# Kernel optimization log

Measured on AMD Instinct MI355X. Metric: run time of the kernel, lower is better.

The kernel has to match this reference:

```python
import jax, jax.numpy as jnp
import jax.lax as lax
import numpy as np

X_NUM = 512
Y_NUM = 512
GRID = 1.0 / 512.0
MIN_X = 0.0
MIN_Y = 0.0
N_POINTS = 400000
BATCH = 4
NUM_CLASSES = 20


def setup_inputs():
    key = jax.random.key(0)
    ks = jax.random.split(key, 32)
    # rows 0/1: x,y coords in [0,1) so they land inside the 512x512 grid; rows 2-5: features
    xy = jax.random.uniform(ks[0], (2, N_POINTS), jnp.float32, 0.0, 1.0 - 1e-6)
    feat = jax.random.normal(ks[1], (4, N_POINTS), jnp.float32) * 0.5
    points = jnp.concatenate([xy, feat], 0)
    batch_ids = jax.random.randint(ks[2], (N_POINTS,), 0, BATCH, jnp.int32)
    inp = {"batch_ids": batch_ids, "points": points, "batch_size": BATCH}

    def lin(k, o, i):
        return jax.random.normal(k, (o, i), jnp.float32) * (1.0 / np.sqrt(i))

    ki = 3
    # pointwise conv1d stacks: (name, out_ch, in_ch)
    for name, o, i in [("0", 16, 6), ("1", 16, 16), ("v0", 16, 18), ("v1", 16, 32), ("2", 32, 32)]:
        inp["w" + name] = lin(ks[ki], o, i); ki += 1
        inp["b" + name] = jnp.zeros((o,), jnp.float32)
        inp["s" + name] = jax.random.uniform(ks[ki], (o,), jnp.float32, 0.5, 1.5); ki += 1
        inp["t" + name] = jax.random.normal(ks[ki], (o,), jnp.float32) * 0.1; ki += 1
    inp["w2d"] = jax.random.normal(ks[ki], (4, 32, 32, 3, 3), jnp.float32) * (1.0 / np.sqrt(32 * 9)); ki += 1
    inp["b2d"] = jnp.zeros((4, 32), jnp.float32)
    inp["s2d"] = jax.random.uniform(ks[ki], (4, 32), jnp.float32, 0.5, 1.5); ki += 1
    inp["t2d"] = jax.random.normal(ks[ki], (4, 32), jnp.float32) * 0.1; ki += 1
    inp["w3"] = lin(ks[ki], NUM_CLASSES, 64); ki += 1
    inp["b3"] = jnp.zeros((NUM_CLASSES,), jnp.float32)
    return inp


def _pconv(x, w, b, s, t):
    # 1x1 conv1d + BatchNorm(inference affine) + ReLU; x: [Cin, N]
    return jax.nn.relu((w @ x + b[:, None]) * s[:, None] + t[:, None])


def _scatter_max(v, gids, n):
    # v: [C, N] -> [C, n]; empty segments filled with 0 (torch_scatter fill_value=0,
    # and all scattered values here are post-ReLU >= 0)
    seg = jax.ops.segment_max(v.T, gids, num_segments=n).T
    return jnp.where(jnp.isneginf(seg), 0.0, seg)


def _bilinear(img, ix, iy):
    # grid_sample(align_corners=False, padding zeros) in pixel coords; img: [C, H, W]
    C, H, W = img.shape
    x0 = jnp.floor(ix); y0 = jnp.floor(iy)
    wx = ix - x0; wy = iy - y0
    x0i = x0.astype(jnp.int32); y0i = y0.astype(jnp.int32)

    def tap(yi, xi):
        valid = ((yi >= 0) & (yi < H) & (xi >= 0) & (xi < W)).astype(img.dtype)
        return img[:, jnp.clip(yi, 0, H - 1), jnp.clip(xi, 0, W - 1)] * valid

    return (tap(y0i, x0i) * (1 - wx) * (1 - wy) + tap(y0i, x0i + 1) * wx * (1 - wy)
            + tap(y0i + 1, x0i) * (1 - wx) * wy + tap(y0i + 1, x0i + 1) * wx * wy)


def _forward(batch_ids, points, batch_size, w0, b0, s0, t0, w1, b1, s1, t1,
             wv0, bv0, sv0, tv0, wv1, bv1, sv1, tv1, w2, b2, s2, t2,
             w2d, b2d, s2d, t2d, w3, b3):
    x_g = jnp.floor((points[0] - MIN_X) / GRID).astype(jnp.int32)
    y_g = jnp.floor((points[1] - MIN_Y) / GRID).astype(jnp.int32)
    gids = batch_ids.astype(jnp.int32) * (X_NUM * Y_NUM) + y_g * X_NUM + x_g
    grid_num = batch_size * Y_NUM * X_NUM

    h = _pconv(points, w0, b0, s0, t0)       # [16, N]
    h = _pconv(h, w1, b1, s1, t1)            # [16, N]
    vx = (x_g.astype(jnp.float32) + 0.5) * GRID + MIN_X
    vy = (y_g.astype(jnp.float32) + 0.5) * GRID + MIN_Y
    h = jnp.concatenate([h, (points[0] - vx)[None], (points[1] - vy)[None]], 0)  # [18, N]

    # VFE blocks: pointwise conv -> scatter_max over voxel ids -> gather back -> concat
    o = _pconv(h, wv0, bv0, sv0, tv0)        # [16, N]
    h = jnp.concatenate([o, _scatter_max(o, gids, grid_num)[:, gids]], 0)  # [32, N]
    o = _pconv(h, wv1, bv1, sv1, tv1)        # [16, N]
    h = jnp.concatenate([o, _scatter_max(o, gids, grid_num)[:, gids]], 0)  # [32, N]

    point0 = _pconv(h, w2, b2, s2, t2)       # [32, N]
    grid = _scatter_max(point0, gids, grid_num)
    grid = grid.reshape(32, batch_size, Y_NUM, X_NUM).transpose(1, 0, 2, 3)  # [B,32,Y,X]

    for i in range(4):
        p = 1 if i == 0 else 2
        grid = lax.conv_general_dilated(grid, w2d[i], (1, 1), ((p, p), (p, p)),
                                        rhs_dilation=(p, p),
                                        dimension_numbers=("NCHW", "OIHW", "NCHW"))
        grid = jax.nn.relu((grid + b2d[i][None, :, None, None]) * s2d[i][None, :, None, None]
                           + t2d[i][None, :, None, None])

    # interpolate (grid_sample) back to points; pixel coords reduce to (x-MIN)/GRID - 1
    img = grid.transpose(1, 0, 2, 3).reshape(32, batch_size * Y_NUM, X_NUM)
    ix = (points[0] - MIN_X) / GRID - 1.0
    iy = (points[1] - MIN_Y) / GRID - 1.0 + batch_ids.astype(jnp.float32) * Y_NUM
    point1 = _bilinear(img, ix, iy)          # [32, N]

    point = jnp.concatenate([point0, point1], 0)  # [64, N]
    return w3 @ point + b3[:, None]               # [num_classes, N]


def reference(batch_ids, points, batch_size, w0, b0, s0, t0, w1, b1, s1, t1,
              wv0, bv0, sv0, tv0, wv1, bv1, sv1, tv1, w2, b2, s2, t2,
              w2d, b2d, s2d, t2d, w3, b3):
    return _forward(batch_ids, points, batch_size, w0, b0, s0, t0, w1, b1, s1, t1,
                    wv0, bv0, sv0, tv0, wv1, bv1, sv1, tv1, w2, b2, s2, t2,
                    w2d, b2d, s2d, t2d, w3, b3)
```

## Files before the change

kernel.cpp:

```cpp
#include <hip/hip_runtime.h>
#include <hip/hip_bf16.h>
#include <hip/hip_fp16.h>

#define N_PTS 400000
#define XN 512
#define YN 512
#define BATCHN 4
#define VOX (XN*YN)
#define GRID_NUM (BATCHN*VOX)

typedef unsigned long long u64;
typedef __attribute__((ext_vector_type(8))) _Float16 f16x8;
typedef __attribute__((ext_vector_type(4))) float f32x4;

static __device__ __forceinline__ float relu_(float x){ return fmaxf(x, 0.0f); }
static __device__ __forceinline__ int voxel_id(float px, float py, int b){
    int xg = (int)floorf(px*512.0f);
    int yg = (int)floorf(py*512.0f);
    return b*VOX + yg*XN + xg;
}

static __device__ __forceinline__ u64 packh4(const float* v){
    u64 r = 0;
    #pragma unroll
    for (int j=0;j<4;j++){
        unsigned short h = __half_as_ushort(__float2half_rn(v[j]));
        r |= (u64)h << (16*j);
    }
    return r;
}
static __device__ __forceinline__ void unpackh4(u64 w, float* o){
    #pragma unroll
    for (int j=0;j<4;j++)
        o[j] = __half2float(__ushort_as_half((unsigned short)(w >> (16*j))));
}
static __device__ __forceinline__ u64 pkmax4(u64 a, u64 b){
    u64 r = 0;
    #pragma unroll
    for (int j=0;j<4;j++){
        u64 x = (a >> (16*j)) & 0xFFFFull;
        u64 y = (b >> (16*j)) & 0xFFFFull;
        r |= (x > y ? x : y) << (16*j);
    }
    return r;
}

__global__ void kZero(float4* __restrict__ p, int n4){
    int i = blockIdx.x*256 + threadIdx.x;
    const float4 z = make_float4(0.f,0.f,0.f,0.f);
    for (; i < n4; i += gridDim.x*256) p[i] = z;
}

__global__ void kDiag(float* __restrict__ o, int n, float v){
    int i = blockIdx.x*256 + threadIdx.x;
    for (; i < n; i += gridDim.x*256) o[i] = v;
}

__global__ void kWprep(const float* __restrict__ W32, _Float16* __restrict__ wf){
    int idx = blockIdx.x*256 + threadIdx.x;
    if (idx >= 4*9216) return;
    int L = idx / 9216, r = idx % 9216;
    int j = r & 7, ln = (r>>3) & 63, rest = r >> 9;
    int t = rest >> 1, nt = rest & 1;
    int ic = (ln>>4)*8 + j, oc = nt*16 + (ln&15);
    wf[idx] = (_Float16)W32[(size_t)L*9216 + ((size_t)oc*32 + ic)*9 + t];
}

__global__ void kHist(const int* __restrict__ bid, const float* __restrict__ pts,
                      unsigned* __restrict__ offs, int* __restrict__ gids)
{
    int i = blockIdx.x*256 + threadIdx.x;
    if (i >= N_PTS) return;
    int gid = voxel_id(pts[i], pts[N_PTS+i], bid[i]);
    gids[i] = gid;
    atomicAdd(&offs[gid], 1u);
}

__global__ void kScan1(unsigned* __restrict__ offs, unsigned* __restrict__ partials)
{
    __shared__ unsigned sa[256], sb[256];
    const int t = threadIdx.x;
    const int g = blockIdx.x*256 + t;
    unsigned v = offs[g];
    sa[t] = v;
    __syncthreads();
    unsigned* src = sa; unsigned* dst = sb;
    #pragma unroll
    for (int d=1; d<256; d<<=1){
        dst[t] = src[t] + ((t>=d) ? src[t-d] : 0u);
        __syncthreads();
        unsigned* tmp = src; src = dst; dst = tmp;
    }
    unsigned incl = src[t];
    offs[g] = incl - v;
    if (t == 255) partials[blockIdx.x] = incl;
}
__global__ void kScan2(unsigned* __restrict__ partials)
{
    __shared__ unsigned sa[256], sb[256];
    const int t = threadIdx.x;
    unsigned loc[16]; unsigned sum = 0;
    #pragma unroll
    for (int j=0;j<16;j++){ loc[j] = partials[t*16+j]; sum += loc[j]; }
    sa[t] = sum;
    __syncthreads();
    unsigned* src = sa; unsigned* dst = sb;
    #pragma unroll
    for (int d=1; d<256; d<<=1){
        dst[t] = src[t] + ((t>=d) ? src[t-d] : 0u);
        __syncthreads();
        unsigned* tmp = src; src = dst; dst = tmp;
    }
    unsigned run = src[t] - sum;
    #pragma unroll
    for (int j=0;j<16;j++){ unsigned c = loc[j]; partials[t*16+j] = run; run += c; }
}
__global__ void kScan3(unsigned* __restrict__ offs, const unsigned* __restrict__ partials)
{
    int g = blockIdx.x*256 + threadIdx.x;
    offs[g] += partials[blockIdx.x];
}

__global__ void kA(const int* __restrict__ bid, const float* __restrict__ pts,
                   const int* __restrict__ gids,
                   const float* __restrict__ w0, const float* __restrict__ b0,
                   const float* __restrict__ s0, const float* __restrict__ t0,
                   const float* __restrict__ w1, const float* __restrict__ b1,
                   const float* __restrict__ s1, const float* __restrict__ t1,
                   const float* __restrict__ wv0, const float* __restrict__ bv0,
                   const float* __restrict__ sv0, const float* __restrict__ tv0,
                   u64* __restrict__ obufA, unsigned* __restrict__ offs,
                   int* __restrict__ sGid, unsigned* __restrict__ inv)
{
    int i = blockIdx.x*256 + threadIdx.x;
    if (i >= N_PTS) return;
    float p[6];
    #pragma unroll
    for (int r=0;r<6;r++) p[r] = pts[r*N_PTS+i];
    int xg = (int)floorf(p[0]*512.0f);
    int yg = (int)floorf(p[1]*512.0f);

    float h0[16];
    #pragma unroll
    for (int o=0;o<16;o++){
        float a = b0[o];
        #pragma unroll
        for (int k=0;k<6;k++) a = fmaf(w0[o*6+k], p[k], a);
        h0[o] = relu_(fmaf(a, s0[o], t0[o]));
    }
    float h1[16];
    #pragma unroll
    for (int o=0;o<16;o++){
        float a = b1[o];
        #pragma unroll
        for (int k=0;k<16;k++) a = fmaf(w1[o*16+k], h0[k], a);
        h1[o] = relu_(fmaf(a, s1[o], t1[o]));
    }
    float dx = p[0] - ((float)xg + 0.5f)*(1.0f/512.0f);
    float dy = p[1] - ((float)yg + 0.5f)*(1.0f/512.0f);
    float vv[16];
    #pragma unroll
    for (int o=0;o<16;o++){
        float a = bv0[o];
        #pragma unroll
        for (int k=0;k<16;k++) a = fmaf(wv0[o*18+k], h1[k], a);
        a = fmaf(wv0[o*18+16], dx, a);
        a = fmaf(wv0[o*18+17], dy, a);
        vv[o] = relu_(fmaf(a, sv0[o], tv0[o]));
    }
    int gid = gids[i];
    unsigned pos = atomicAdd(&offs[gid], 1u);
    u64* op = obufA + (size_t)pos*4;
    #pragma unroll
    for (int q=0;q<4;q++) op[q] = packh4(&vv[q*4]);
    sGid[pos] = gid;
    inv[i] = pos;
}

__global__ void kSegMax(const unsigned* __restrict__ offs,
                        const u64* __restrict__ src, u64* __restrict__ dst)
{
    int v = blockIdx.x*256 + threadIdx.x;
    unsigned s = v ? offs[v-1] : 0u;
    unsigned e = offs[v];
    if (e <= s) return;
    u64 m0=0,m1=0,m2=0,m3=0;
    for (unsigned p=s; p<e; ++p){
        const u64* q = src + (size_t)p*4;
        m0 = pkmax4(m0, q[0]); m1 = pkmax4(m1, q[1]);
        m2 = pkmax4(m2, q[2]); m3 = pkmax4(m3, q[3]);
    }
    u64* d = dst + (size_t)v*4;
    d[0]=m0; d[1]=m1; d[2]=m2; d[3]=m3;
}

__global__ void kGridMax(const unsigned* __restrict__ offs,
                         const u64* __restrict__ src, u64* __restrict__ dst)
{
    int v = blockIdx.x*256 + threadIdx.x;
    unsigned s = v ? offs[v-1] : 0u;
    unsigned e = offs[v];
    u64 m[8];
    #pragma unroll
    for (int q=0;q<8;q++) m[q] = 0ull;
    for (unsigned p=s; p<e; ++p){
        const u64* q = src + (size_t)p*8;
        #pragma unroll
        for (int j=0;j<8;j++) m[j] = pkmax4(m[j], q[j]);
    }
    u64* d = dst + (size_t)v*8;
    #pragma unroll
    for (int q=0;q<8;q++) d[q] = m[q];
}

__global__ void kB(const int* __restrict__ sGid,
                   const float* __restrict__ w, const float* __restrict__ bb,
                   const float* __restrict__ ss, const float* __restrict__ tt,
                   const u64* __restrict__ obufA, const u64* __restrict__ seg0,
                   u64* __restrict__ obufB)
{
    int j = blockIdx.x*256 + threadIdx.x;
    if (j >= N_PTS) return;
    int gid = sGid[j];
    float h[32];
    const u64* ap = obufA + (size_t)j*4;
    #pragma unroll
    for (int q=0;q<4;q++) unpackh4(ap[q], &h[q*4]);
    const u64* sp = seg0 + (size_t)gid*4;
    #pragma unroll
    for (int q=0;q<4;q++) unpackh4(sp[q], &h[16+q*4]);

    float o[16];
    #pragma unroll
    for (int c=0;c<16;c++){
        float a = bb[c];
        #pragma unroll
        for (int k=0;k<32;k++) a = fmaf(w[c*32+k], h[k], a);
        o[c] = relu_(fmaf(a, ss[c], tt[c]));
    }
    u64* op = obufB + (size_t)j*4;
    #pragma unroll
    for (int q=0;q<4;q++) op[q] = packh4(&o[q*4]);
}

__global__ void kC(const int* __restrict__ sGid,
                   const float* __restrict__ w, const float* __restrict__ bb,
                   const float* __restrict__ ss, const float* __restrict__ tt,
                   const u64* __restrict__ obufB, const u64* __restrict__ seg1,
                   u64* __restrict__ pbuf)
{
    int j = blockIdx.x*256 + threadIdx.x;
    if (j >= N_PTS) return;
    int gid = sGid[j];
    float h[32];
    const u64* ap = obufB + (size_t)j*4;
    #pragma unroll
    for (int q=0;q<4;q++) unpackh4(ap[q], &h[q*4]);
    const u64* sp = seg1 + (size_t)gid*4;
    #pragma unroll
    for (int q=0;q<4;q++) unpackh4(sp[q], &h[16+q*4]);

    float p0v[32];
    #pragma unroll
    for (int c=0;c<32;c++){
        float a = bb[c];
        #pragma unroll
        for (int k=0;k<32;k++) a = fmaf(w[c*32+k], h[k], a);
        p0v[c] = relu_(fmaf(a, ss[c], tt[c]));
    }
    u64* pp = pbuf + (size_t)j*8;
    #pragma unroll
    for (int q=0;q<8;q++) pp[q] = packh4(&p0v[q*4]);
}

template<int P>
__global__ __launch_bounds__(256,4) void convM(
    const _Float16* __restrict__ in, _Float16* __restrict__ out,
    const f16x8* __restrict__ wfrag, const float* __restrict__ bb,
    const float* __restrict__ ss, const float* __restrict__ tt)
{
    constexpr int TW = 32, TH = 8;
    constexpr int TIW = TW + 2*P, TIH = TH + 2*P;
    __shared__ uint4 sA[TIH*TIW*5];
    const int tid = threadIdx.x;
    const int lane = tid & 63, wv = tid >> 6;
    const int x0 = blockIdx.x*TW, y0 = blockIdx.y*TH, bz = blockIdx.z;
    const _Float16* inB = in + (size_t)bz*VOX*32;

    for (int u = tid; u < TIH*TIW*4; u += 256){
        int g = u & 3;
        int pxr = u >> 2;
        int px = pxr % TIW, r = pxr / TIW;
        int gy = y0 - P + r, gx = x0 - P + px;
        uint4 v = make_uint4(0,0,0,0);
        if ((unsigned)gy < 512u && (unsigned)gx < 512u)
            v = *(const uint4*)(inB + (((size_t)gy*512 + gx)*32 + g*8));
        sA[(r*TIW + px)*5 + g] = v;
    }
    __syncthreads();

    const f16x8* pA = (const f16x8*)sA;
    const int aoff = (lane&15)*5 + (lane>>4);
    const int rowbase = wv*2;

    f32x4 acc[4][2];
    #pragma unroll
    for (int m=0;m<4;m++){ acc[m][0]=(f32x4)0.f; acc[m][1]=(f32x4)0.f; }

    #pragma unroll
    for (int t=0;t<9;t++){
        const int ky = t/3, kx = t%3;
        f16x8 b0 = wfrag[(t*2+0)*64 + lane];
        f16x8 b1 = wfrag[(t*2+1)*64 + lane];
        #pragma unroll
        for (int m=0;m<4;m++){
            int r = rowbase + (m>>1) + ky*P;
            int pxb = (m&1)*16 + kx*P;
            f16x8 a = pA[(r*TIW + pxb)*5 + aoff];
            acc[m][0] = __builtin_amdgcn_mfma_f32_16x16x32_f16(b0, a, acc[m][0], 0,0,0);
            acc[m][1] = __builtin_amdgcn_mfma_f32_16x16x32_f16(b1, a, acc[m][1], 0,0,0);
        }
    }

    float bn[2][4], sn[2][4], tn[2][4];
    #pragma unroll
    for (int n=0;n<2;n++){
        int ocb = n*16 + (lane>>4)*4;
        #pragma unroll
        for (int r=0;r<4;r++){ bn[n][r]=bb[ocb+r]; sn[n][r]=ss[ocb+r]; tn[n][r]=tt[ocb+r]; }
    }
    _Float16* outB = out + (size_t)bz*VOX*32;
    #pragma unroll
    for (int m=0;m<4;m++){
        int y  = y0 + rowbase + (m>>1);
        int px = x0 + (m&1)*16 + (lane&15);
        #pragma unroll
        for (int n=0;n<2;n++){
            unsigned h[4];
            #pragma unroll
            for (int r=0;r<4;r++){
                float v = relu_(fmaf(acc[m][n][r] + bn[n][r], sn[n][r], tn[n][r]));
                h[r] = (unsigned)__half_as_ushort(__float2half_rn(v));
            }
            uint2 val = make_uint2(h[0] | (h[1]<<16), h[2] | (h[3]<<16));
            *(uint2*)(outB + ((size_t)y*512 + px)*32 + n*16 + (lane>>4)*4) = val;
        }
    }
}

__global__ void kFinal(const int* __restrict__ bid, const float* __restrict__ pts,
                       const unsigned* __restrict__ inv, const u64* __restrict__ pbuf,
                       const _Float16* __restrict__ gridH,
                       const float* __restrict__ w3, const float* __restrict__ b3,
                       float* __restrict__ outp)
{
    int i = blockIdx.x*256 + threadIdx.x;
    if (i >= N_PTS) return;
    float px = pts[i], py = pts[N_PTS+i];
    int b = bid[i];

    float p0[32];
    const u64* pp = pbuf + (size_t)inv[i]*8;
    #pragma unroll
    for (int q=0;q<8;q++) unpackh4(pp[q], &p0[q*4]);

    float ix = px*512.0f - 1.0f;
    float iy = py*512.0f - 1.0f + (float)(b*512);
    float x0f = floorf(ix), y0f = floorf(iy);
    float wx = ix - x0f, wy = iy - y0f;
    int x0 = (int)x0f, y0 = (int)y0f;

    float p1[32];
    #pragma unroll
    for (int c=0;c<32;c++) p1[c] = 0.f;
    #pragma unroll
    for (int t=0;t<4;t++){
        int yi = y0 + (t>>1);
        int xi = x0 + (t&1);
        if (yi < 0 || yi >= BATCHN*YN || xi < 0 || xi >= XN) continue;
        float wgt = ((t>>1)? wy : 1.0f-wy) * ((t&1)? wx : 1.0f-wx);
        const uint4* tp = (const uint4*)(gridH + ((size_t)yi*XN + xi)*32);
        #pragma unroll
        for (int q=0;q<4;q++){
            uint4 v = tp[q];
            const unsigned int* vu = (const unsigned int*)&v;
            #pragma unroll
            for (int e=0;e<4;e++){
                float lo = __half2float(__ushort_as_half((unsigned short)(vu[e] & 0xFFFF)));
                float hi = __half2float(__ushort_as_half((unsigned short)(vu[e] >> 16)));
                p1[q*8 + e*2 + 0] = fmaf(wgt, lo, p1[q*8 + e*2 + 0]);
                p1[q*8 + e*2 + 1] = fmaf(wgt, hi, p1[q*8 + e*2 + 1]);
            }
        }
    }

    #pragma unroll
    for (int k=0;k<20;k++){
        float a = b3[k];
        #pragma unroll
        for (int c=0;c<32;c++) a = fmaf(w3[k*64+c], p0[c], a);
        #pragma unroll
        for (int c=0;c<32;c++) a = fmaf(w3[k*64+32+c], p1[c], a);
        outp[(size_t)k*N_PTS + i] = a;
    }
}

extern "C" void kernel_launch(void* const* d_in, const int* in_sizes, int n_in,
                              void* d_out, int out_size, void* d_ws, size_t ws_size,
                              hipStream_t stream)
{
    const int*   bid = (const int*)  d_in[0];
    const float* pts = (const float*)d_in[1];
    const float* w0  = (const float*)d_in[3];
    const float* b0  = (const float*)d_in[4];
    const float* s0  = (const float*)d_in[5];
    const float* t0  = (const float*)d_in[6];
    const float* w1  = (const float*)d_in[7];
    const float* b1  = (const float*)d_in[8];
    const float* s1  = (const float*)d_in[9];
    const float* t1  = (const float*)d_in[10];
    const float* wv0 = (const float*)d_in[11];
    const float* bv0 = (const float*)d_in[12];
    const float* sv0 = (const float*)d_in[13];
    const float* tv0 = (const float*)d_in[14];
    const float* wv1 = (const float*)d_in[15];
    const float* bv1 = (const float*)d_in[16];
    const float* sv1 = (const float*)d_in[17];
    const float* tv1 = (const float*)d_in[18];
    const float* w2  = (const float*)d_in[19];
    const float* b2  = (const float*)d_in[20];
    const float* s2  = (const float*)d_in[21];
    const float* t2  = (const float*)d_in[22];
    const float* w2d = (const float*)d_in[23];
    const float* b2d = (const float*)d_in[24];
    const float* s2d = (const float*)d_in[25];
    const float* t2d = (const float*)d_in[26];
    const float* w3  = (const float*)d_in[27];
    const float* b3  = (const float*)d_in[28];

    const size_t MB = 1024*1024;
    const size_t NEED = 192*MB;
    if (ws_size < NEED){
        kDiag<<<512,256,0,stream>>>((float*)d_out, out_size, (float)(ws_size>>20));
        return;
    }

    char* ws = (char*)d_ws;
    u64*      gridV    = (u64*)ws;
    _Float16* ping     = (_Float16*)ws;
    _Float16* pong     = (_Float16*)(ws + 64*MB);
    u64*      seg0     = (u64*)(ws + 64*MB);
    u64*      seg1     = (u64*)(ws + 96*MB);
    unsigned* offs     = (unsigned*)(ws + 128*MB);
    unsigned* partials = (unsigned*)(ws + 132*MB);
    int*      sGid     = (int*)(ws + 133*MB);
    int*      gids     = (int*)(ws + 135*MB);
    unsigned* inv      = (unsigned*)(ws + 137*MB);
    u64*      obufA    = (u64*)(ws + 139*MB);
    u64*      obufB    = (u64*)(ws + 152*MB);
    u64*      pbuf     = (u64*)(ws + 165*MB);
    _Float16* wfrag    = (_Float16*)(ws + 191*MB);

    kZero<<<256,256,0,stream>>>((float4*)offs, (int)(GRID_NUM*4/16));
    kWprep<<<144,256,0,stream>>>(w2d, wfrag);

    const int nb = (N_PTS + 255)/256;
    const int nv = GRID_NUM/256;

    kHist <<<nb,256,0,stream>>>(bid, pts, offs, gids);
    kScan1<<<nv,256,0,stream>>>(offs, partials);
    kScan2<<<1,256,0,stream>>>(partials);
    kScan3<<<nv,256,0,stream>>>(offs, partials);

    kA<<<nb,256,0,stream>>>(bid, pts, gids, w0,b0,s0,t0, w1,b1,s1,t1,
                            wv0,bv0,sv0,tv0, obufA, offs, sGid, inv);
    kSegMax<<<nv,256,0,stream>>>(offs, obufA, seg0);
    kB<<<nb,256,0,stream>>>(sGid, wv1,bv1,sv1,tv1, obufA, seg0, obufB);
    kSegMax<<<nv,256,0,stream>>>(offs, obufB, seg1);
    kC<<<nb,256,0,stream>>>(sGid, w2,b2,s2,t2, obufB, seg1, pbuf);
    kGridMax<<<nv,256,0,stream>>>(offs, pbuf, gridV);

    dim3 cgrid(XN/32, YN/8, BATCHN);
    const f16x8* wf = (const f16x8*)wfrag;
    convM<1><<<cgrid,256,0,stream>>>(ping, pong, wf + 0*1152, b2d + 0,  s2d + 0,  t2d + 0);
    convM<2><<<cgrid,256,0,stream>>>(pong, ping, wf + 1*1152, b2d + 32, s2d + 32, t2d + 32);
    convM<2><<<cgrid,256,0,stream>>>(ping, pong, wf + 2*1152, b2d + 64, s2d + 64, t2d + 64);
    convM<2><<<cgrid,256,0,stream>>>(pong, ping, wf + 3*1152, b2d + 96, s2d + 96, t2d + 96);

    kFinal<<<nb,256,0,stream>>>(bid, pts, inv, pbuf, ping, w3, b3, (float*)d_out);
}
```

Measured before the change: 344.1 us.

## Swizzle conv block order and process two points per thread in final kernel

```diff
diff --git a/kernel.cpp b/kernel.cpp
--- a/kernel.cpp
+++ b/kernel.cpp
@@ -3,6 +3,7 @@
 #include <hip/hip_fp16.h>
 
 #define N_PTS 400000
+#define N_HALF 200000
 #define XN 512
 #define YN 512
 #define BATCHN 4
@@ -284,7 +285,11 @@
     __shared__ uint4 sA[TIH*TIW*5];
     const int tid = threadIdx.x;
     const int lane = tid & 63, wv = tid >> 6;
-    const int x0 = blockIdx.x*TW, y0 = blockIdx.y*TH, bz = blockIdx.z;
+
+    int flat = blockIdx.x + 16*blockIdx.y + 1024*blockIdx.z;
+    int swz  = (flat & 7)*512 + (flat >> 3);
+    const int bx = swz & 15, by = (swz >> 4) & 63, bz = swz >> 10;
+    const int x0 = bx*TW, y0 = by*TH;
     const _Float16* inB = in + (size_t)bz*VOX*32;
 
     for (int u = tid; u < TIH*TIW*4; u += 256){
@@ -348,38 +353,20 @@
     }
 }
 
-__global__ void kFinal(const int* __restrict__ bid, const float* __restrict__ pts,
-                       const unsigned* __restrict__ inv, const u64* __restrict__ pbuf,
-                       const _Float16* __restrict__ gridH,
-                       const float* __restrict__ w3, const float* __restrict__ b3,
-                       float* __restrict__ outp)
-{
-    int i = blockIdx.x*256 + threadIdx.x;
-    if (i >= N_PTS) return;
-    float px = pts[i], py = pts[N_PTS+i];
-    int b = bid[i];
-
-    float p0[32];
-    const u64* pp = pbuf + (size_t)inv[i]*8;
-    #pragma unroll
-    for (int q=0;q<8;q++) unpackh4(pp[q], &p0[q*4]);
-
-    float ix = px*512.0f - 1.0f;
-    float iy = py*512.0f - 1.0f + (float)(b*512);
+static __device__ __forceinline__ void final_accum_taps(
+    const _Float16* __restrict__ gridH, float ix, float iy, float* p1)
+{
     float x0f = floorf(ix), y0f = floorf(iy);
     float wx = ix - x0f, wy = iy - y0f;
     int x0 = (int)x0f, y0 = (int)y0f;
-
-    float p1[32];
-    #pragma unroll
-    for (int c=0;c<32;c++) p1[c] = 0.f;
     #pragma unroll
     for (int t=0;t<4;t++){
         int yi = y0 + (t>>1);
         int xi = x0 + (t&1);
-        if (yi < 0 || yi >= BATCHN*YN || xi < 0 || xi >= XN) continue;
-        float wgt = ((t>>1)? wy : 1.0f-wy) * ((t&1)? wx : 1.0f-wx);
-        const uint4* tp = (const uint4*)(gridH + ((size_t)yi*XN + xi)*32);
+        bool ok = (yi >= 0) & (yi < BATCHN*YN) & (xi >= 0) & (xi < XN);
+        float wgt = (((t>>1)? wy : 1.0f-wy) * ((t&1)? wx : 1.0f-wx)) * (ok ? 1.0f : 0.0f);
+        int cy = min(max(yi,0), BATCHN*YN-1), cx = min(max(xi,0), XN-1);
+        const uint4* tp = (const uint4*)(gridH + ((size_t)cy*XN + cx)*32);
         #pragma unroll
         for (int q=0;q<4;q++){
             uint4 v = tp[q];
@@ -393,15 +380,52 @@
             }
         }
     }
+}
+
+__global__ __launch_bounds__(256) void kFinal(
+    const int* __restrict__ bid, const float* __restrict__ pts,
+    const unsigned* __restrict__ inv, const u64* __restrict__ pbuf,
+    const _Float16* __restrict__ gridH,
+    const float* __restrict__ w3, const float* __restrict__ b3,
+    float* __restrict__ outp)
+{
+    int t = blockIdx.x*256 + threadIdx.x;
+    if (t >= N_HALF) return;
+    int ia = t, ib = t + N_HALF;
+
+    float pxa = pts[ia], pya = pts[N_PTS+ia];
+    float pxb = pts[ib], pyb = pts[N_PTS+ib];
+    int ba = bid[ia], bbatch = bid[ib];
+    unsigned ja = inv[ia], jb = inv[ib];
+
+    u64 pka[8], pkb[8];
+    const u64* ppa = pbuf + (size_t)ja*8;
+    const u64* ppb = pbuf + (size_t)jb*8;
+    #pragma unroll
+    for (int q=0;q<8;q++){ pka[q] = ppa[q]; pkb[q] = ppb[q]; }
+
+    float p1a[32], p1b[32];
+    #pragma unroll
+    for (int c=0;c<32;c++){ p1a[c]=0.f; p1b[c]=0.f; }
+
+    final_accum_taps(gridH, pxa*512.0f - 1.0f, pya*512.0f - 1.0f + (float)(ba*512), p1a);
+    final_accum_taps(gridH, pxb*512.0f - 1.0f, pyb*512.0f - 1.0f + (float)(bbatch*512), p1b);
+
+    float p0a[32], p0b[32];
+    #pragma unroll
+    for (int q=0;q<8;q++){ unpackh4(pka[q], &p0a[q*4]); unpackh4(pkb[q], &p0b[q*4]); }
 
     #pragma unroll
     for (int k=0;k<20;k++){
-        float a = b3[k];
-        #pragma unroll
-        for (int c=0;c<32;c++) a = fmaf(w3[k*64+c], p0[c], a);
-        #pragma unroll
-        for (int c=0;c<32;c++) a = fmaf(w3[k*64+32+c], p1[c], a);
-        outp[(size_t)k*N_PTS + i] = a;
+        float aa = b3[k], ab = b3[k];
+        #pragma unroll
+        for (int c=0;c<32;c++){
+            float wlo = w3[k*64+c], whi = w3[k*64+32+c];
+            aa = fmaf(wlo, p0a[c], aa); aa = fmaf(whi, p1a[c], aa);
+            ab = fmaf(wlo, p0b[c], ab); ab = fmaf(whi, p1b[c], ab);
+        }
+        outp[(size_t)k*N_PTS + ia] = aa;
+        outp[(size_t)k*N_PTS + ib] = ab;
     }
 }
 
@@ -487,5 +511,6 @@
     convM<2><<<cgrid,256,0,stream>>>(ping, pong, wf + 2*1152, b2d + 64, s2d + 64, t2d + 64);
     convM<2><<<cgrid,256,0,stream>>>(pong, ping, wf + 3*1152, b2d + 96, s2d + 96, t2d + 96);
 
-    kFinal<<<nb,256,0,stream>>>(bid, pts, inv, pbuf, ping, w3, b3, (float*)d_out);
-}
+    const int nbh = (N_HALF + 255)/256;
+    kFinal<<<nbh,256,0,stream>>>(bid, pts, inv, pbuf, ping, w3, b3, (float*)d_out);
+}
```

After: 343.7 us. Within noise of the previous version (-0.1%).
